# Kernel tuning notes

Hardware: AMD Instinct MI355X
Metric: run time of the kernel (lower is better)

The kernel has to match this reference:

```python
import jax, jax.numpy as jnp
import numpy as np

N_NODES = 100000
N_EDGES = 1600000
D_IN = 128
D_HID = 128
D_OUT = 128
N_GRAPHS = 64


def setup_inputs() -> dict:
    key = jax.random.key(0)
    ks = jax.random.split(key, 10)
    x = jax.random.normal(ks[0], (N_NODES, D_IN), dtype=jnp.float32)
    edge_index = jax.random.randint(ks[1], (2, N_EDGES), 0, N_NODES, dtype=jnp.int64)
    graph_id = jnp.sort(jax.random.randint(ks[2], (N_NODES,), 0, N_GRAPHS, dtype=jnp.int64))
    s1 = 1.0 / np.sqrt(D_IN)
    s2 = 1.0 / np.sqrt(D_HID)
    s3 = 1.0 / np.sqrt(D_OUT)
    W1 = jax.random.normal(ks[3], (D_IN, D_HID), dtype=jnp.float32) * s1
    b1 = jnp.zeros((D_HID,), dtype=jnp.float32)
    W2 = jax.random.normal(ks[4], (D_HID, D_OUT), dtype=jnp.float32) * s2
    b2 = jnp.zeros((D_OUT,), dtype=jnp.float32)
    Wr1 = jax.random.normal(ks[5], (D_OUT, D_OUT), dtype=jnp.float32) * s3
    br1 = jnp.zeros((D_OUT,), dtype=jnp.float32)
    Wr2 = jax.random.normal(ks[6], (D_OUT, D_OUT), dtype=jnp.float32) * s3
    br2 = jnp.zeros((D_OUT,), dtype=jnp.float32)
    return {"x": x, "edge_index": edge_index, "graph_id": graph_id,
            "num_graphs": N_GRAPHS, "W1": W1, "b1": b1, "W2": W2, "b2": b2,
            "Wr1": Wr1, "br1": br1, "Wr2": Wr2, "br2": br2}


def _graph_conv(h, W, b, src, dst, norm_src, norm_dst, n_nodes):
    # DGL GraphConv, norm='both': out = D_dst^{-1/2} A (D_src^{-1/2} h) W + b
    h = h * norm_src[:, None]
    h = h @ W  # project first (cheap, keeps SpMM on the smaller/equal dim)
    agg = jax.ops.segment_sum(h[src], dst, num_segments=n_nodes)
    return agg * norm_dst[:, None] + b


def reference(x, edge_index, graph_id, num_graphs, W1, b1, W2, b2, Wr1, br1, Wr2, br2):
    src, dst = edge_index[0], edge_index[1]
    n_nodes = x.shape[0]
    ones = jnp.ones((src.shape[0],), dtype=x.dtype)
    deg_out = jax.ops.segment_sum(ones, src, num_segments=n_nodes)
    deg_in = jax.ops.segment_sum(ones, dst, num_segments=n_nodes)
    norm_src = jnp.clip(deg_out, 1.0) ** -0.5
    norm_dst = jnp.clip(deg_in, 1.0) ** -0.5

    # layer 1 + relu (dropout is identity in eval mode)
    h = _graph_conv(x, W1, b1, src, dst, norm_src, norm_dst, n_nodes)
    h = jax.nn.relu(h)
    # layer 2 + relu
    h = _graph_conv(h, W2, b2, src, dst, norm_src, norm_dst, n_nodes)
    h = jax.nn.relu(h)

    # per-graph mean pooling (dgl.mean_nodes)
    sums = jax.ops.segment_sum(h, graph_id, num_segments=num_graphs)
    counts = jax.ops.segment_sum(jnp.ones((n_nodes,), dtype=h.dtype), graph_id,
                                 num_segments=num_graphs)
    hg = sums / jnp.clip(counts, 1.0)[:, None]

    # readout MLP: Linear -> ReLU -> Linear
    out = jax.nn.relu(hg @ Wr1 + br1) @ Wr2 + br2
    return (out, h)
```

## Files before the change

kernel.cpp:

```cpp
#include <hip/hip_runtime.h>
#include <math.h>


#define D 128
#define BSH 8
#define BKT 256
#define CAP 4608
#define SCHUNK 3200

typedef _Float16 half8 __attribute__((ext_vector_type(8)));
typedef _Float16 half4v __attribute__((ext_vector_type(4)));
typedef _Float16 half2v __attribute__((ext_vector_type(2)));
typedef float f32x4 __attribute__((ext_vector_type(4)));

union H8 { half8 v; half2v h[4]; };

__global__ __launch_bounds__(512) void k_build(const int* __restrict__ src,
                                               const int* __restrict__ dst,
                                               int* __restrict__ cnt_d,
                                               int* __restrict__ cnt_s,
                                               int* __restrict__ packed_d,
                                               int* __restrict__ packed_s,
                                               int E, int nbkt) {
  __shared__ int es[SCHUNK], ed[SCHUNK];
  __shared__ int hd[512], hs[512], based[512], bases[512];
  int t = threadIdx.x;
  hd[t] = 0; hs[t] = 0;
  __syncthreads();
  int chunk = (E + gridDim.x - 1) / gridDim.x;
  int lo = blockIdx.x * chunk, hi = min(lo + chunk, E);
  int n = hi - lo;
  for (int i = t; i < n; i += 512) {
    int s = src[lo + i], d = dst[lo + i];
    es[i] = s; ed[i] = d;
    atomicAdd(&hd[d >> BSH], 1);
    atomicAdd(&hs[s >> BSH], 1);
  }
  __syncthreads();
  int cD = (t < nbkt) ? hd[t] : 0;
  int cS = (t < nbkt) ? hs[t] : 0;
  __syncthreads();
  hd[t] = 0; hs[t] = 0;
  if (t < nbkt) {
    based[t] = cD ? atomicAdd(&cnt_d[t], cD) : 0;
    bases[t] = cS ? atomicAdd(&cnt_s[t], cS) : 0;
  }
  __syncthreads();
  for (int i = t; i < n; i += 512) {
    int s = es[i], d = ed[i];
    int b1 = d >> BSH;
    int p1 = based[b1] + atomicAdd(&hd[b1], 1);
    if (p1 < CAP) packed_d[b1 * CAP + p1] = ((d & (BKT - 1)) << 17) | s;
    int b2 = s >> BSH;
    int p2 = bases[b2] + atomicAdd(&hs[b2], 1);
    if (p2 < CAP) packed_s[b2 * CAP + p2] = s & (BKT - 1);
  }
}

__global__ __launch_bounds__(512) void k_fine(const int* __restrict__ packed_d,
                                              const int* __restrict__ cnt_d,
                                              int* __restrict__ row_lo,
                                              int* __restrict__ row_hi,
                                              int* __restrict__ csr,
                                              const int* __restrict__ packed_s,
                                              const int* __restrict__ cnt_s,
                                              float* __restrict__ norm_src,
                                              int N, int nbkt) {
  __shared__ int hist[256];
  int t = threadIdx.x;
  if (blockIdx.x >= nbkt) {
    int b = blockIdx.x - nbkt;
    int lo = b * CAP;
    int cnt = min(cnt_s[b], CAP);
    if (t < 256) hist[t] = 0;
    __syncthreads();
    for (int e = t; e < cnt; e += 512)
      atomicAdd(&hist[packed_s[lo + e]], 1);
    __syncthreads();
    int nbase = b << BSH;
    if (t < 256 && nbase + t < N)
      norm_src[nbase + t] = rsqrtf(fmaxf((float)hist[t], 1.0f));
    return;
  }
  __shared__ int excl[256];
  __shared__ int ecache[CAP];
  __shared__ int sorted[CAP];
  int b = blockIdx.x;
  int lo = b * CAP;
  int cnt = min(cnt_d[b], CAP);
  if (t < 256) hist[t] = 0;
  __syncthreads();
  for (int e = t; e < cnt; e += 512) {
    int p = packed_d[lo + e];
    ecache[e] = p;
    atomicAdd(&hist[p >> 17], 1);
  }
  __syncthreads();
  int v = (t < 256) ? hist[t] : 0;
  for (int off = 1; off < 256; off <<= 1) {
    int a = (t >= off && t < 256) ? hist[t - off] : 0;
    __syncthreads();
    if (t < 256) hist[t] += a;
    __syncthreads();
  }
  int nbase = b << BSH;
  if (t < 256) {
    excl[t] = hist[t] - v;
    if (nbase + t < N) {
      row_lo[nbase + t] = lo + hist[t] - v;
      row_hi[nbase + t] = lo + hist[t];
    }
  }
  __syncthreads();
  if (t < 256) hist[t] = 0;
  __syncthreads();
  for (int e = t; e < cnt; e += 512) {
    int p = ecache[e];
    int dlow = p >> 17;
    int r = atomicAdd(&hist[dlow], 1);
    sorted[excl[dlow] + r] = p & 0x1FFFF;
  }
  __syncthreads();
  for (int e = t; e < cnt; e += 512)
    csr[lo + e] = sorted[e];
}

__global__ __launch_bounds__(256) void k_prep(const float* __restrict__ W1,
                                              const float* __restrict__ W2,
                                              _Float16* __restrict__ Wt1,
                                              _Float16* __restrict__ Wt2,
                                              int* __restrict__ cnt_d,
                                              float* __restrict__ pool,
                                              const int* __restrict__ gid,
                                              int* __restrict__ gptr, int N) {
  if (blockIdx.x == 128) {
    int t = threadIdx.x;
    cnt_d[t] = 0; cnt_d[t + 256] = 0; cnt_d[t + 512] = 0; cnt_d[t + 768] = 0;
    for (int i = t; i < 64 * D; i += 256) pool[i] = 0.0f;
    if (t <= 64) {
      int lo = 0, hi = N;
      while (lo < hi) {
        int m = (lo + hi) >> 1;
        if (gid[m] < t) lo = m + 1; else hi = m;
      }
      gptr[t] = lo;
    }
    return;
  }
  int idx = blockIdx.x * 256 + threadIdx.x;
  int m = idx >> 14;
  int i = idx & 16383;
  int k = i >> 7, n = i & 127;
  const float* W = m ? W2 : W1;
  _Float16* Wt = m ? Wt2 : Wt1;
  Wt[n * 128 + k] = (_Float16)W[i];
}

__global__ __launch_bounds__(256) void k_gemm1(const float* __restrict__ A,
                                               const _Float16* __restrict__ Wt,
                                               const float* __restrict__ scale,
                                               _Float16* __restrict__ C, int N) {
  __shared__ _Float16 As[64][136];
  __shared__ _Float16 Cs[64][128];
  const int r0 = blockIdx.x * 64;
  const int t = threadIdx.x;
  for (int i = t; i < 64 * 32; i += 256) {
    int r = i >> 5, c4 = i & 31;
    float4 v = {0.f, 0.f, 0.f, 0.f};
    if (r0 + r < N) {
      v = ((const float4*)A)[(size_t)(r0 + r) * 32 + c4];
      float s = scale[r0 + r];
      v.x *= s; v.y *= s; v.z *= s; v.w *= s;
    }
    half4v h = {(_Float16)v.x, (_Float16)v.y, (_Float16)v.z, (_Float16)v.w};
    *(half4v*)&As[r][c4 * 4] = h;
  }
  __syncthreads();
  const int w = t >> 6, l = t & 63;
  const int c = l & 15, quad = l >> 4;
  f32x4 acc[8];
#pragma unroll
  for (int nt = 0; nt < 8; ++nt) acc[nt] = (f32x4){0.f, 0.f, 0.f, 0.f};
#pragma unroll
  for (int kc = 0; kc < 4; ++kc) {
    half8 a = *(const half8*)&As[w * 16 + c][kc * 32 + quad * 8];
#pragma unroll
    for (int nt = 0; nt < 8; ++nt) {
      half8 b = *(const half8*)&Wt[(size_t)(nt * 16 + c) * 128 + kc * 32 + quad * 8];
      acc[nt] = __builtin_amdgcn_mfma_f32_16x16x32_f16(a, b, acc[nt], 0, 0, 0);
    }
  }
#pragma unroll
  for (int nt = 0; nt < 8; ++nt)
#pragma unroll
    for (int r = 0; r < 4; ++r)
      Cs[w * 16 + quad * 4 + r][nt * 16 + c] = (_Float16)acc[nt][r];
  __syncthreads();
  for (int i = t; i < 64 * 16; i += 256) {
    int r = i >> 4, c8 = i & 15;
    if (r0 + r < N)
      ((half8*)C)[(size_t)(r0 + r) * 16 + c8] = *(half8*)&Cs[r][c8 * 8];
  }
}

__global__ __launch_bounds__(256) void k_gemm2(const _Float16* __restrict__ A,
                                               const _Float16* __restrict__ Wt,
                                               _Float16* __restrict__ C, int N) {
  __shared__ _Float16 As[64][136];
  __shared__ _Float16 Cs[64][128];
  const int r0 = blockIdx.x * 64;
  const int t = threadIdx.x;
  for (int i = t; i < 64 * 16; i += 256) {
    int r = i >> 4, c8 = i & 15;
    half8 v = {0, 0, 0, 0, 0, 0, 0, 0};
    if (r0 + r < N) v = ((const half8*)A)[(size_t)(r0 + r) * 16 + c8];
    *(half8*)&As[r][c8 * 8] = v;
  }
  __syncthreads();
  const int w = t >> 6, l = t & 63;
  const int c = l & 15, quad = l >> 4;
  f32x4 acc[8];
#pragma unroll
  for (int nt = 0; nt < 8; ++nt) acc[nt] = (f32x4){0.f, 0.f, 0.f, 0.f};
#pragma unroll
  for (int kc = 0; kc < 4; ++kc) {
    half8 a = *(const half8*)&As[w * 16 + c][kc * 32 + quad * 8];
#pragma unroll
    for (int nt = 0; nt < 8; ++nt) {
      half8 b = *(const half8*)&Wt[(size_t)(nt * 16 + c) * 128 + kc * 32 + quad * 8];
      acc[nt] = __builtin_amdgcn_mfma_f32_16x16x32_f16(a, b, acc[nt], 0, 0, 0);
    }
  }
#pragma unroll
  for (int nt = 0; nt < 8; ++nt)
#pragma unroll
    for (int r = 0; r < 4; ++r)
      Cs[w * 16 + quad * 4 + r][nt * 16 + c] = (_Float16)acc[nt][r];
  __syncthreads();
  for (int i = t; i < 64 * 16; i += 256) {
    int r = i >> 4, c8 = i & 15;
    if (r0 + r < N)
      ((half8*)C)[(size_t)(r0 + r) * 16 + c8] = *(half8*)&Cs[r][c8 * 8];
  }
}

#define PK_ROW(u)                                                           \
  _Pragma("unroll")                                                         \
  for (int k = 0; k < 4; ++k) acch[k] += (u).h[k];

__device__ __forceinline__ void gather_core(const half8* __restrict__ P8,
                                            const int* __restrict__ csr,
                                            int start, int end, int cg, int eg,
                                            int lane, float* acc) {
  half2v acch[4] = {{(_Float16)0.f, (_Float16)0.f}, {(_Float16)0.f, (_Float16)0.f},
                    {(_Float16)0.f, (_Float16)0.f}, {(_Float16)0.f, (_Float16)0.f}};
  for (int s0 = start; s0 < end; s0 += 64) {
    int cnt = min(64, end - s0);
    int idx = (s0 + lane < end) ? csr[s0 + lane] : 0;
    int base = 0;
    for (; base + 16 <= cnt; base += 16) {
      int i0 = __shfl(idx, base + eg);
      int i1 = __shfl(idx, base + 4 + eg);
      int i2 = __shfl(idx, base + 8 + eg);
      int i3 = __shfl(idx, base + 12 + eg);
      H8 u0, u1, u2, u3;
      u0.v = P8[(size_t)i0 * 16 + cg];
      u1.v = P8[(size_t)i1 * 16 + cg];
      u2.v = P8[(size_t)i2 * 16 + cg];
      u3.v = P8[(size_t)i3 * 16 + cg];
      PK_ROW(u0) PK_ROW(u1) PK_ROW(u2) PK_ROW(u3)
    }
    for (; base + 4 <= cnt; base += 4) {
      int i0 = __shfl(idx, base + eg);
      H8 u0;
      u0.v = P8[(size_t)i0 * 16 + cg];
      PK_ROW(u0)
    }
    if (base < cnt) {
      int j = min(base + eg, cnt - 1);
      int i0 = __shfl(idx, j);
      if (base + eg < cnt) {
        H8 u0;
        u0.v = P8[(size_t)i0 * 16 + cg];
        PK_ROW(u0)
      }
    }
  }
#pragma unroll
  for (int k = 0; k < 4; ++k) {
    acc[2 * k]     = (float)acch[k].x;
    acc[2 * k + 1] = (float)acch[k].y;
  }
#pragma unroll
  for (int j = 0; j < 8; ++j) {
    acc[j] += __shfl_xor(acc[j], 16);
    acc[j] += __shfl_xor(acc[j], 32);
  }
}

__global__ __launch_bounds__(256) void k_gather1(const half8* __restrict__ P8,
                                                 const int* __restrict__ row_lo,
                                                 const int* __restrict__ row_hi,
                                                 const int* __restrict__ csr,
                                                 const float* __restrict__ bias,
                                                 const float* __restrict__ norm_src,
                                                 half2v* __restrict__ outH, int N) {
  int wid = (blockIdx.x * 256 + threadIdx.x) >> 6;
  if (wid >= N) return;
  int lane = threadIdx.x & 63;
  int cg = lane & 15, eg = lane >> 4;
  int start = row_lo[wid], end = row_hi[wid];
  float acc[8];
  gather_core(P8, csr, start, end, cg, eg, lane, acc);
  float nd = rsqrtf(fmaxf((float)(end - start), 1.0f));
  float ns = norm_src[wid];
  float2 b = ((const float2*)bias)[cg * 4 + eg];
  half2v o = {(_Float16)(fmaxf(acc[eg * 2] * nd + b.x, 0.f) * ns),
              (_Float16)(fmaxf(acc[eg * 2 + 1] * nd + b.y, 0.f) * ns)};
  outH[(size_t)wid * 64 + cg * 4 + eg] = o;
}

__global__ __launch_bounds__(256) void k_gather2(const half8* __restrict__ P8,
                                                 const int* __restrict__ row_lo,
                                                 const int* __restrict__ row_hi,
                                                 const int* __restrict__ csr,
                                                 const float* __restrict__ bias,
                                                 float2* __restrict__ outH, int N) {
  int wid = (blockIdx.x * 256 + threadIdx.x) >> 6;
  if (wid >= N) return;
  int lane = threadIdx.x & 63;
  int cg = lane & 15, eg = lane >> 4;
  int start = row_lo[wid], end = row_hi[wid];
  float acc[8];
  gather_core(P8, csr, start, end, cg, eg, lane, acc);
  float nd = rsqrtf(fmaxf((float)(end - start), 1.0f));
  float2 b = ((const float2*)bias)[cg * 4 + eg];
  float2 o;
  o.x = fmaxf(acc[eg * 2] * nd + b.x, 0.f);
  o.y = fmaxf(acc[eg * 2 + 1] * nd + b.y, 0.f);
  outH[(size_t)wid * 64 + cg * 4 + eg] = o;
}

__global__ __launch_bounds__(256) void k_pool(const float* __restrict__ H,
                                              const int* __restrict__ gptr,
                                              float* __restrict__ pool) {
  int g = blockIdx.x >> 3, chunk = blockIdx.x & 7;
  int col = threadIdx.x & 127, rpar = threadIdx.x >> 7;
  int s = gptr[g], e = gptr[g + 1];
  float acc = 0.0f;
  for (int r = s + chunk * 2 + rpar; r < e; r += 16)
    acc += H[(size_t)r * D + col];
  __shared__ float red[256];
  red[threadIdx.x] = acc;
  __syncthreads();
  if (rpar == 0) atomicAdd(&pool[g * D + col], acc + red[threadIdx.x + 128]);
}

__global__ __launch_bounds__(128) void k_readout(const float* __restrict__ pool,
                                                 const int* __restrict__ gptr,
                                                 const float* __restrict__ Wr1,
                                                 const float* __restrict__ br1,
                                                 const float* __restrict__ Wr2,
                                                 const float* __restrict__ br2,
                                                 float* __restrict__ out) {
  int g = blockIdx.x;
  int j = threadIdx.x;
  __shared__ float hg[D];
  __shared__ float t1[D];
  float cnt = fmaxf((float)(gptr[g + 1] - gptr[g]), 1.0f);
  hg[j] = pool[(size_t)g * D + j] / cnt;
  __syncthreads();
  float a = br1[j];
  for (int k = 0; k < D; ++k) a += hg[k] * Wr1[(size_t)k * D + j];
  t1[j] = fmaxf(a, 0.0f);
  __syncthreads();
  float b = br2[j];
  for (int k = 0; k < D; ++k) b += t1[k] * Wr2[(size_t)k * D + j];
  out[(size_t)g * D + j] = b;
}

extern "C" void kernel_launch(void* const* d_in, const int* in_sizes, int n_in,
                              void* d_out, int out_size, void* d_ws, size_t ws_size,
                              hipStream_t stream) {
  const float* x   = (const float*)d_in[0];
  const int* edge  = (const int*)d_in[1];
  const int* gid   = (const int*)d_in[2];
  const float* W1  = (const float*)d_in[4];
  const float* b1  = (const float*)d_in[5];
  const float* W2  = (const float*)d_in[6];
  const float* b2  = (const float*)d_in[7];
  const float* Wr1 = (const float*)d_in[8];
  const float* br1 = (const float*)d_in[9];
  const float* Wr2 = (const float*)d_in[10];
  const float* br2 = (const float*)d_in[11];

  const int N = in_sizes[0] / D;
  const int E = in_sizes[1] / 2;
  const int* src = edge;
  const int* dst = edge + E;
  const int nbkt = (N + BKT - 1) >> BSH;

  float* bufA     = (float*)d_ws;
  float* bufB     = bufA + (size_t)N * D;
  int* row_lo     = (int*)(bufB + (size_t)N * D);
  int* row_hi     = row_lo + N;
  int* csr        = row_hi + N;
  float* norm_src = (float*)(csr + (size_t)nbkt * CAP);
  float* pool     = norm_src + N;
  int* gptr       = (int*)(pool + 64 * D);
  int* cnt_d      = gptr + 65;
  int* cnt_s      = cnt_d + 512;
  _Float16* Wt1   = (_Float16*)(cnt_s + 512);
  _Float16* Wt2   = Wt1 + 128 * 128;
  int* packed_d   = (int*)bufA;
  int* packed_s   = packed_d + (size_t)nbkt * CAP;
  size_t need = ((size_t)2 * N * D + 3 * (size_t)N + (size_t)nbkt * CAP
                 + 64 * D + 65 + 1024 + 16384 + 1024) * sizeof(float);
  if (ws_size < need) return;

  float* out_g = (float*)d_out;
  float* h_out = out_g + 64 * D;

  _Float16* P   = (_Float16*)bufA;
  _Float16* h1p = (_Float16*)bufB;

  k_prep<<<129, 256, 0, stream>>>(W1, W2, Wt1, Wt2, cnt_d, pool, gid, gptr, N);

  const int build_grid = (E + SCHUNK - 1) / SCHUNK;
  k_build<<<build_grid, 512, 0, stream>>>(src, dst, cnt_d, cnt_s,
                                          packed_d, packed_s, E, nbkt);
  k_fine<<<2 * nbkt, 512, 0, stream>>>(packed_d, cnt_d, row_lo, row_hi, csr,
                                       packed_s, cnt_s, norm_src, N, nbkt);

  const int gemm_grid = (N + 63) / 64;

  k_gemm1<<<gemm_grid, 256, 0, stream>>>(x, Wt1, norm_src, P, N);
  k_gather1<<<(N * 64 + 255) / 256, 256, 0, stream>>>(
      (const half8*)P, row_lo, row_hi, csr, b1, norm_src, (half2v*)h1p, N);

  k_gemm2<<<gemm_grid, 256, 0, stream>>>(h1p, Wt2, P, N);
  k_gather2<<<(N * 64 + 255) / 256, 256, 0, stream>>>(
      (const half8*)P, row_lo, row_hi, csr, b2, (float2*)h_out, N);

  k_pool<<<64 * 8, 256, 0, stream>>>(h_out, gptr, pool);
  k_readout<<<64, 128, 0, stream>>>(pool, gptr, Wr1, br1, Wr2, br2, out_g);
}
```

Before: 383.3 us.

## Merge graph build and first GEMM into cooperative persistent kernel; fuse pool+readout

Replaces the prep, bucket-build, fine-sort and first GEMM launches with one cooperative persistent kernel that uses grid-wide syncs between phases and a shared-memory union. Pooling and the readout MLP are likewise merged into one cooperative kernel. The aim is to cut kernel launch gaps and tail effects across several small phases. The cost is that phases now run at a limited grid size (at most 1024 blocks of 256 threads instead of 512-thread blocks). Grid syncs and reduced parallelism in the build and sort steps could make those phases slower.

```diff
diff --git a/kernel.cpp b/kernel.cpp
--- a/kernel.cpp
+++ b/kernel.cpp
@@ -1,4 +1,5 @@
 #include <hip/hip_runtime.h>
+#include <hip/hip_cooperative_groups.h>
 #include <math.h>
 
 
@@ -6,7 +7,6 @@
 #define BSH 8
 #define BKT 256
 #define CAP 4608
-#define SCHUNK 3200
 
 typedef _Float16 half8 __attribute__((ext_vector_type(8)));
 typedef _Float16 half4v __attribute__((ext_vector_type(4)));
@@ -15,127 +15,38 @@
 
 union H8 { half8 v; half2v h[4]; };
 
-__global__ __launch_bounds__(512) void k_build(const int* __restrict__ src,
-                                               const int* __restrict__ dst,
-                                               int* __restrict__ cnt_d,
-                                               int* __restrict__ cnt_s,
-                                               int* __restrict__ packed_d,
-                                               int* __restrict__ packed_s,
-                                               int E, int nbkt) {
-  __shared__ int es[SCHUNK], ed[SCHUNK];
-  __shared__ int hd[512], hs[512], based[512], bases[512];
-  int t = threadIdx.x;
-  hd[t] = 0; hs[t] = 0;
-  __syncthreads();
-  int chunk = (E + gridDim.x - 1) / gridDim.x;
-  int lo = blockIdx.x * chunk, hi = min(lo + chunk, E);
-  int n = hi - lo;
-  for (int i = t; i < n; i += 512) {
-    int s = src[lo + i], d = dst[lo + i];
-    es[i] = s; ed[i] = d;
-    atomicAdd(&hd[d >> BSH], 1);
-    atomicAdd(&hs[s >> BSH], 1);
-  }
-  __syncthreads();
-  int cD = (t < nbkt) ? hd[t] : 0;
-  int cS = (t < nbkt) ? hs[t] : 0;
-  __syncthreads();
-  hd[t] = 0; hs[t] = 0;
-  if (t < nbkt) {
-    based[t] = cD ? atomicAdd(&cnt_d[t], cD) : 0;
-    bases[t] = cS ? atomicAdd(&cnt_s[t], cS) : 0;
-  }
-  __syncthreads();
-  for (int i = t; i < n; i += 512) {
-    int s = es[i], d = ed[i];
-    int b1 = d >> BSH;
-    int p1 = based[b1] + atomicAdd(&hd[b1], 1);
-    if (p1 < CAP) packed_d[b1 * CAP + p1] = ((d & (BKT - 1)) << 17) | s;
-    int b2 = s >> BSH;
-    int p2 = bases[b2] + atomicAdd(&hs[b2], 1);
-    if (p2 < CAP) packed_s[b2 * CAP + p2] = s & (BKT - 1);
-  }
-}
-
-__global__ __launch_bounds__(512) void k_fine(const int* __restrict__ packed_d,
-                                              const int* __restrict__ cnt_d,
-                                              int* __restrict__ row_lo,
-                                              int* __restrict__ row_hi,
-                                              int* __restrict__ csr,
-                                              const int* __restrict__ packed_s,
-                                              const int* __restrict__ cnt_s,
-                                              float* __restrict__ norm_src,
-                                              int N, int nbkt) {
-  __shared__ int hist[256];
-  int t = threadIdx.x;
-  if (blockIdx.x >= nbkt) {
-    int b = blockIdx.x - nbkt;
-    int lo = b * CAP;
-    int cnt = min(cnt_s[b], CAP);
-    if (t < 256) hist[t] = 0;
-    __syncthreads();
-    for (int e = t; e < cnt; e += 512)
-      atomicAdd(&hist[packed_s[lo + e]], 1);
-    __syncthreads();
-    int nbase = b << BSH;
-    if (t < 256 && nbase + t < N)
-      norm_src[nbase + t] = rsqrtf(fmaxf((float)hist[t], 1.0f));
-    return;
-  }
-  __shared__ int excl[256];
-  __shared__ int ecache[CAP];
-  __shared__ int sorted[CAP];
-  int b = blockIdx.x;
-  int lo = b * CAP;
-  int cnt = min(cnt_d[b], CAP);
-  if (t < 256) hist[t] = 0;
-  __syncthreads();
-  for (int e = t; e < cnt; e += 512) {
-    int p = packed_d[lo + e];
-    ecache[e] = p;
-    atomicAdd(&hist[p >> 17], 1);
-  }
-  __syncthreads();
-  int v = (t < 256) ? hist[t] : 0;
-  for (int off = 1; off < 256; off <<= 1) {
-    int a = (t >= off && t < 256) ? hist[t - off] : 0;
-    __syncthreads();
-    if (t < 256) hist[t] += a;
-    __syncthreads();
-  }
-  int nbase = b << BSH;
-  if (t < 256) {
-    excl[t] = hist[t] - v;
-    if (nbase + t < N) {
-      row_lo[nbase + t] = lo + hist[t] - v;
-      row_hi[nbase + t] = lo + hist[t];
-    }
-  }
-  __syncthreads();
-  if (t < 256) hist[t] = 0;
-  __syncthreads();
-  for (int e = t; e < cnt; e += 512) {
-    int p = ecache[e];
-    int dlow = p >> 17;
-    int r = atomicAdd(&hist[dlow], 1);
-    sorted[excl[dlow] + r] = p & 0x1FFFF;
-  }
-  __syncthreads();
-  for (int e = t; e < cnt; e += 512)
-    csr[lo + e] = sorted[e];
-}
-
-__global__ __launch_bounds__(256) void k_prep(const float* __restrict__ W1,
-                                              const float* __restrict__ W2,
-                                              _Float16* __restrict__ Wt1,
-                                              _Float16* __restrict__ Wt2,
-                                              int* __restrict__ cnt_d,
-                                              float* __restrict__ pool,
-                                              const int* __restrict__ gid,
-                                              int* __restrict__ gptr, int N) {
-  if (blockIdx.x == 128) {
-    int t = threadIdx.x;
-    cnt_d[t] = 0; cnt_d[t + 256] = 0; cnt_d[t + 512] = 0; cnt_d[t + 768] = 0;
+union BigLds {
+  struct { int hd[512], hs[512], based[512], bases[512]; } b;
+  struct { int hist[256], excl[256], ecache[CAP], sorted[CAP]; } f;
+  struct { int hist[256]; } fs;
+  struct { _Float16 As[64][136]; _Float16 Cs[64][128]; } g;
+};
+
+__global__ __launch_bounds__(256, 4) void k_graph(
+    const float* __restrict__ W1, const float* __restrict__ W2,
+    _Float16* __restrict__ Wt1, _Float16* __restrict__ Wt2,
+    int* __restrict__ cnt_d, int* __restrict__ cnt_s,
+    float* __restrict__ pool, const int* __restrict__ gid,
+    int* __restrict__ gptr,
+    const int* __restrict__ src, const int* __restrict__ dst,
+    int* __restrict__ packed_d, int* __restrict__ packed_s,
+    int* __restrict__ row_lo, int* __restrict__ row_hi,
+    int* __restrict__ csr, float* __restrict__ norm_src,
+    const float* __restrict__ x, _Float16* __restrict__ P,
+    int N, int E, int nbkt) {
+  __shared__ BigLds sh;
+  cooperative_groups::grid_group grid = cooperative_groups::this_grid();
+  const int t = threadIdx.x;
+  const int bid = blockIdx.x;
+  const int G = gridDim.x;
+
+  for (int idx = bid * 256 + t; idx < 2 * 128 * 128; idx += G * 256) {
+    int m = idx >> 14, i = idx & 16383;
+    int k = i >> 7, n = i & 127;
+    (m ? Wt2 : Wt1)[n * 128 + k] = (_Float16)((m ? W2 : W1)[i]);
+  }
+  if (bid == 0) {
+    for (int i = t; i < 1024; i += 256) cnt_d[i] = 0;
     for (int i = t; i < 64 * D; i += 256) pool[i] = 0.0f;
     if (t <= 64) {
       int lo = 0, hi = N;
@@ -145,61 +56,187 @@
       }
       gptr[t] = lo;
     }
-    return;
-  }
-  int idx = blockIdx.x * 256 + threadIdx.x;
-  int m = idx >> 14;
-  int i = idx & 16383;
-  int k = i >> 7, n = i & 127;
-  const float* W = m ? W2 : W1;
-  _Float16* Wt = m ? Wt2 : Wt1;
-  Wt[n * 128 + k] = (_Float16)W[i];
-}
-
-__global__ __launch_bounds__(256) void k_gemm1(const float* __restrict__ A,
-                                               const _Float16* __restrict__ Wt,
-                                               const float* __restrict__ scale,
-                                               _Float16* __restrict__ C, int N) {
-  __shared__ _Float16 As[64][136];
-  __shared__ _Float16 Cs[64][128];
-  const int r0 = blockIdx.x * 64;
+  }
+  grid.sync();
+
+  {
+    sh.b.hd[t] = 0; sh.b.hd[t + 256] = 0;
+    sh.b.hs[t] = 0; sh.b.hs[t + 256] = 0;
+    __syncthreads();
+    int chunk = (E + G - 1) / G;
+    int lo = bid * chunk, hi = min(lo + chunk, E);
+    for (int i = lo + t; i < hi; i += 256) {
+      atomicAdd(&sh.b.hd[dst[i] >> BSH], 1);
+      atomicAdd(&sh.b.hs[src[i] >> BSH], 1);
+    }
+    __syncthreads();
+    int c0d = sh.b.hd[t], c1d = sh.b.hd[t + 256];
+    int c0s = sh.b.hs[t], c1s = sh.b.hs[t + 256];
+    __syncthreads();
+    sh.b.hd[t] = 0; sh.b.hd[t + 256] = 0;
+    sh.b.hs[t] = 0; sh.b.hs[t + 256] = 0;
+    if (t < nbkt)       sh.b.based[t]       = c0d ? atomicAdd(&cnt_d[t], c0d) : 0;
+    if (t + 256 < nbkt) sh.b.based[t + 256] = c1d ? atomicAdd(&cnt_d[t + 256], c1d) : 0;
+    if (t < nbkt)       sh.b.bases[t]       = c0s ? atomicAdd(&cnt_s[t], c0s) : 0;
+    if (t + 256 < nbkt) sh.b.bases[t + 256] = c1s ? atomicAdd(&cnt_s[t + 256], c1s) : 0;
+    __syncthreads();
+    for (int i = lo + t; i < hi; i += 256) {
+      int s = src[i], d = dst[i];
+      int b1 = d >> BSH;
+      int p1 = sh.b.based[b1] + atomicAdd(&sh.b.hd[b1], 1);
+      if (p1 < CAP) packed_d[b1 * CAP + p1] = ((d & (BKT - 1)) << 17) | s;
+      int b2 = s >> BSH;
+      int p2 = sh.b.bases[b2] + atomicAdd(&sh.b.hs[b2], 1);
+      if (p2 < CAP) packed_s[b2 * CAP + p2] = s & (BKT - 1);
+    }
+  }
+  grid.sync();
+
+  for (int task = bid; task < 2 * nbkt; task += G) {
+    if (task >= nbkt) {
+      int b = task - nbkt;
+      int lo = b * CAP;
+      int cnt = min(cnt_s[b], CAP);
+      sh.fs.hist[t] = 0;
+      __syncthreads();
+      for (int e = t; e < cnt; e += 256)
+        atomicAdd(&sh.fs.hist[packed_s[lo + e]], 1);
+      __syncthreads();
+      int nbase = b << BSH;
+      if (nbase + t < N)
+        norm_src[nbase + t] = rsqrtf(fmaxf((float)sh.fs.hist[t], 1.0f));
+      __syncthreads();
+    } else {
+      int b = task;
+      int lo = b * CAP;
+      int cnt = min(cnt_d[b], CAP);
+      sh.f.hist[t] = 0;
+      __syncthreads();
+      for (int e = t; e < cnt; e += 256) {
+        int p = packed_d[lo + e];
+        sh.f.ecache[e] = p;
+        atomicAdd(&sh.f.hist[p >> 17], 1);
+      }
+      __syncthreads();
+      int v = sh.f.hist[t];
+      for (int off = 1; off < 256; off <<= 1) {
+        int a = (t >= off) ? sh.f.hist[t - off] : 0;
+        __syncthreads();
+        sh.f.hist[t] += a;
+        __syncthreads();
+      }
+      sh.f.excl[t] = sh.f.hist[t] - v;
+      int nbase = b << BSH;
+      if (nbase + t < N) {
+        row_lo[nbase + t] = lo + sh.f.hist[t] - v;
+        row_hi[nbase + t] = lo + sh.f.hist[t];
+      }
+      __syncthreads();
+      sh.f.hist[t] = 0;
+      __syncthreads();
+      for (int e = t; e < cnt; e += 256) {
+        int p = sh.f.ecache[e];
+        int dlow = p >> 17;
+        int r = atomicAdd(&sh.f.hist[dlow], 1);
+        sh.f.sorted[sh.f.excl[dlow] + r] = p & 0x1FFFF;
+      }
+      __syncthreads();
+      for (int e = t; e < cnt; e += 256)
+        csr[lo + e] = sh.f.sorted[e];
+      __syncthreads();
+    }
+  }
+  grid.sync();
+
+  {
+    const int ntiles = (N + 63) >> 6;
+    const int w = t >> 6, l = t & 63;
+    const int c = l & 15, quad = l >> 4;
+    for (int tile = bid; tile < ntiles; tile += G) {
+      const int r0 = tile * 64;
+      for (int i = t; i < 64 * 32; i += 256) {
+        int r = i >> 5, c4 = i & 31;
+        float4 v = {0.f, 0.f, 0.f, 0.f};
+        if (r0 + r < N) {
+          v = ((const float4*)x)[(size_t)(r0 + r) * 32 + c4];
+          float s = norm_src[r0 + r];
+          v.x *= s; v.y *= s; v.z *= s; v.w *= s;
+        }
+        half4v h = {(_Float16)v.x, (_Float16)v.y, (_Float16)v.z, (_Float16)v.w};
+        *(half4v*)&sh.g.As[r][c4 * 4] = h;
+      }
+      __syncthreads();
+      f32x4 acc[8];
+#pragma unroll
+      for (int nt = 0; nt < 8; ++nt) acc[nt] = (f32x4){0.f, 0.f, 0.f, 0.f};
+#pragma unroll
+      for (int kc = 0; kc < 4; ++kc) {
+        half8 a = *(const half8*)&sh.g.As[w * 16 + c][kc * 32 + quad * 8];
+#pragma unroll
+        for (int nt = 0; nt < 8; ++nt) {
+          half8 b = *(const half8*)&Wt1[(size_t)(nt * 16 + c) * 128 + kc * 32 + quad * 8];
+          acc[nt] = __builtin_amdgcn_mfma_f32_16x16x32_f16(a, b, acc[nt], 0, 0, 0);
+        }
+      }
+#pragma unroll
+      for (int nt = 0; nt < 8; ++nt)
+#pragma unroll
+        for (int r = 0; r < 4; ++r)
+          sh.g.Cs[w * 16 + quad * 4 + r][nt * 16 + c] = (_Float16)acc[nt][r];
+      __syncthreads();
+      for (int i = t; i < 64 * 16; i += 256) {
+        int r = i >> 4, c8 = i & 15;
+        if (r0 + r < N)
+          ((half8*)P)[(size_t)(r0 + r) * 16 + c8] = *(half8*)&sh.g.Cs[r][c8 * 8];
+      }
+      __syncthreads();
+    }
+  }
+}
+
+__global__ __launch_bounds__(256, 2) void k_tail(
+    const float* __restrict__ H, const int* __restrict__ gptr,
+    float* __restrict__ pool,
+    const float* __restrict__ Wr1, const float* __restrict__ br1,
+    const float* __restrict__ Wr2, const float* __restrict__ br2,
+    float* __restrict__ out) {
+  cooperative_groups::grid_group grid = cooperative_groups::this_grid();
   const int t = threadIdx.x;
-  for (int i = t; i < 64 * 32; i += 256) {
-    int r = i >> 5, c4 = i & 31;
-    float4 v = {0.f, 0.f, 0.f, 0.f};
-    if (r0 + r < N) {
-      v = ((const float4*)A)[(size_t)(r0 + r) * 32 + c4];
-      float s = scale[r0 + r];
-      v.x *= s; v.y *= s; v.z *= s; v.w *= s;
-    }
-    half4v h = {(_Float16)v.x, (_Float16)v.y, (_Float16)v.z, (_Float16)v.w};
-    *(half4v*)&As[r][c4 * 4] = h;
-  }
-  __syncthreads();
-  const int w = t >> 6, l = t & 63;
-  const int c = l & 15, quad = l >> 4;
-  f32x4 acc[8];
-#pragma unroll
-  for (int nt = 0; nt < 8; ++nt) acc[nt] = (f32x4){0.f, 0.f, 0.f, 0.f};
-#pragma unroll
-  for (int kc = 0; kc < 4; ++kc) {
-    half8 a = *(const half8*)&As[w * 16 + c][kc * 32 + quad * 8];
-#pragma unroll
-    for (int nt = 0; nt < 8; ++nt) {
-      half8 b = *(const half8*)&Wt[(size_t)(nt * 16 + c) * 128 + kc * 32 + quad * 8];
-      acc[nt] = __builtin_amdgcn_mfma_f32_16x16x32_f16(a, b, acc[nt], 0, 0, 0);
-    }
-  }
-#pragma unroll
-  for (int nt = 0; nt < 8; ++nt)
-#pragma unroll
-    for (int r = 0; r < 4; ++r)
-      Cs[w * 16 + quad * 4 + r][nt * 16 + c] = (_Float16)acc[nt][r];
-  __syncthreads();
-  for (int i = t; i < 64 * 16; i += 256) {
-    int r = i >> 4, c8 = i & 15;
-    if (r0 + r < N)
-      ((half8*)C)[(size_t)(r0 + r) * 16 + c8] = *(half8*)&Cs[r][c8 * 8];
+  const int bid = blockIdx.x;
+  const int G = gridDim.x;
+  __shared__ float red[256];
+  __shared__ float hg[128];
+  __shared__ float t1[128];
+
+  for (int task = bid; task < 512; task += G) {
+    int g = task >> 3, chunk = task & 7;
+    int col = t & 127, rpar = t >> 7;
+    int s = gptr[g], e = gptr[g + 1];
+    float acc = 0.0f;
+    for (int r = s + chunk * 2 + rpar; r < e; r += 16)
+      acc += H[(size_t)r * D + col];
+    red[t] = acc;
+    __syncthreads();
+    if (rpar == 0) atomicAdd(&pool[g * D + col], acc + red[t + 128]);
+    __syncthreads();
+  }
+  grid.sync();
+  for (int g = bid; g < 64; g += G) {
+    float cnt = fmaxf((float)(gptr[g + 1] - gptr[g]), 1.0f);
+    if (t < 128) hg[t] = pool[(size_t)g * D + t] / cnt;
+    __syncthreads();
+    if (t < 128) {
+      float a = br1[t];
+      for (int k = 0; k < D; ++k) a += hg[k] * Wr1[(size_t)k * D + t];
+      t1[t] = fmaxf(a, 0.0f);
+    }
+    __syncthreads();
+    if (t < 128) {
+      float b = br2[t];
+      for (int k = 0; k < D; ++k) b += t1[k] * Wr2[(size_t)k * D + t];
+      out[(size_t)g * D + t] = b;
+    }
+    __syncthreads();
   }
 }
 
@@ -341,44 +378,6 @@
   outH[(size_t)wid * 64 + cg * 4 + eg] = o;
 }
 
-__global__ __launch_bounds__(256) void k_pool(const float* __restrict__ H,
-                                              const int* __restrict__ gptr,
-                                              float* __restrict__ pool) {
-  int g = blockIdx.x >> 3, chunk = blockIdx.x & 7;
-  int col = threadIdx.x & 127, rpar = threadIdx.x >> 7;
-  int s = gptr[g], e = gptr[g + 1];
-  float acc = 0.0f;
-  for (int r = s + chunk * 2 + rpar; r < e; r += 16)
-    acc += H[(size_t)r * D + col];
-  __shared__ float red[256];
-  red[threadIdx.x] = acc;
-  __syncthreads();
-  if (rpar == 0) atomicAdd(&pool[g * D + col], acc + red[threadIdx.x + 128]);
-}
-
-__global__ __launch_bounds__(128) void k_readout(const float* __restrict__ pool,
-                                                 const int* __restrict__ gptr,
-                                                 const float* __restrict__ Wr1,
-                                                 const float* __restrict__ br1,
-                                                 const float* __restrict__ Wr2,
-                                                 const float* __restrict__ br2,
-                                                 float* __restrict__ out) {
-  int g = blockIdx.x;
-  int j = threadIdx.x;
-  __shared__ float hg[D];
-  __shared__ float t1[D];
-  float cnt = fmaxf((float)(gptr[g + 1] - gptr[g]), 1.0f);
-  hg[j] = pool[(size_t)g * D + j] / cnt;
-  __syncthreads();
-  float a = br1[j];
-  for (int k = 0; k < D; ++k) a += hg[k] * Wr1[(size_t)k * D + j];
-  t1[j] = fmaxf(a, 0.0f);
-  __syncthreads();
-  float b = br2[j];
-  for (int k = 0; k < D; ++k) b += t1[k] * Wr2[(size_t)k * D + j];
-  out[(size_t)g * D + j] = b;
-}
-
 extern "C" void kernel_launch(void* const* d_in, const int* in_sizes, int n_in,
                               void* d_out, int out_size, void* d_ws, size_t ws_size,
                               hipStream_t stream) {
@@ -424,24 +423,44 @@
   _Float16* P   = (_Float16*)bufA;
   _Float16* h1p = (_Float16*)bufB;
 
-  k_prep<<<129, 256, 0, stream>>>(W1, W2, Wt1, Wt2, cnt_d, pool, gid, gptr, N);
-
-  const int build_grid = (E + SCHUNK - 1) / SCHUNK;
-  k_build<<<build_grid, 512, 0, stream>>>(src, dst, cnt_d, cnt_s,
-                                          packed_d, packed_s, E, nbkt);
-  k_fine<<<2 * nbkt, 512, 0, stream>>>(packed_d, cnt_d, row_lo, row_hi, csr,
-                                       packed_s, cnt_s, norm_src, N, nbkt);
-
-  const int gemm_grid = (N + 63) / 64;
-
-  k_gemm1<<<gemm_grid, 256, 0, stream>>>(x, Wt1, norm_src, P, N);
+  static int G1 = 0, G2 = 0;
+  if (G1 == 0) {
+    int occ1 = 0, occ2 = 0, ncu = 256;
+    hipOccupancyMaxActiveBlocksPerMultiprocessor(&occ1, k_graph, 256, 0);
+    hipOccupancyMaxActiveBlocksPerMultiprocessor(&occ2, k_tail, 256, 0);
+    hipDeviceProp_t prop;
+    int dev = 0;
+    if (hipGetDevice(&dev) == hipSuccess &&
+        hipGetDeviceProperties(&prop, dev) == hipSuccess &&
+        prop.multiProcessorCount > 0)
+      ncu = prop.multiProcessorCount;
+    G1 = (occ1 > 0) ? min(1024, occ1 * ncu) : 1024;
+    G2 = (occ2 > 0) ? min(512, occ2 * ncu) : 512;
+  }
+
+  {
+    int n_ = N, e_ = E, nb_ = nbkt;
+    void* args[] = {
+      (void*)&W1, (void*)&W2, (void*)&Wt1, (void*)&Wt2,
+      (void*)&cnt_d, (void*)&cnt_s, (void*)&pool, (void*)&gid, (void*)&gptr,
+      (void*)&src, (void*)&dst, (void*)&packed_d, (void*)&packed_s,
+      (void*)&row_lo, (void*)&row_hi, (void*)&csr, (void*)&norm_src,
+      (void*)&x, (void*)&P, (void*)&n_, (void*)&e_, (void*)&nb_};
+    hipLaunchCooperativeKernel(k_graph, dim3(G1), dim3(256), args, 0, stream);
+  }
+
   k_gather1<<<(N * 64 + 255) / 256, 256, 0, stream>>>(
       (const half8*)P, row_lo, row_hi, csr, b1, norm_src, (half2v*)h1p, N);
 
+  const int gemm_grid = (N + 63) / 64;
   k_gemm2<<<gemm_grid, 256, 0, stream>>>(h1p, Wt2, P, N);
   k_gather2<<<(N * 64 + 255) / 256, 256, 0, stream>>>(
       (const half8*)P, row_lo, row_hi, csr, b2, (float2*)h_out, N);
 
-  k_pool<<<64 * 8, 256, 0, stream>>>(h_out, gptr, pool);
-  k_readout<<<64, 128, 0, stream>>>(pool, gptr, Wr1, br1, Wr2, br2, out_g);
-}
+  {
+    void* args[] = {
+      (void*)&h_out, (void*)&gptr, (void*)&pool,
+      (void*)&Wr1, (void*)&br1, (void*)&Wr2, (void*)&br2, (void*)&out_g};
+    hipLaunchCooperativeKernel(k_tail, dim3(G2), dim3(256), args, 0, stream);
+  }
+}
```

After: 681.2 us. +77.7%, slower.

## Fold weight prep into edge-binning kernel and drop shared edge staging

Applied to the files above, without the earlier changes.

Removes the separate k_prep launch. Its work moves into k_build: the weight transpose to fp16 and the graph-pointer binary search. The counter and pool zeroing becomes hipMemsetAsync calls. k_build now runs a fixed grid of 1024 blocks of 256 threads and reads src/dst twice from global memory, where before it staged about 3200 edges per block in LDS. The aim is to cut one launch and the LDS pressure that limited occupancy. The cost is a second global read of the edge arrays and two extra memset operations.

```diff
diff --git a/kernel.cpp b/kernel.cpp
--- a/kernel.cpp
+++ b/kernel.cpp
@@ -6,7 +6,7 @@
 #define BSH 8
 #define BKT 256
 #define CAP 4608
-#define SCHUNK 3200
+#define BGRID 1024
 
 typedef _Float16 half8 __attribute__((ext_vector_type(8)));
 typedef _Float16 half4v __attribute__((ext_vector_type(4)));
@@ -15,39 +15,59 @@
 
 union H8 { half8 v; half2v h[4]; };
 
-__global__ __launch_bounds__(512) void k_build(const int* __restrict__ src,
+__global__ __launch_bounds__(256) void k_build(const int* __restrict__ src,
                                                const int* __restrict__ dst,
                                                int* __restrict__ cnt_d,
                                                int* __restrict__ cnt_s,
                                                int* __restrict__ packed_d,
                                                int* __restrict__ packed_s,
-                                               int E, int nbkt) {
-  __shared__ int es[SCHUNK], ed[SCHUNK];
+                                               const float* __restrict__ W1,
+                                               const float* __restrict__ W2,
+                                               _Float16* __restrict__ Wt1,
+                                               _Float16* __restrict__ Wt2,
+                                               const int* __restrict__ gid,
+                                               int* __restrict__ gptr,
+                                               int N, int E, int nbkt) {
   __shared__ int hd[512], hs[512], based[512], bases[512];
-  int t = threadIdx.x;
-  hd[t] = 0; hs[t] = 0;
+  const int t = threadIdx.x;
+  const int bid = blockIdx.x;
+
+  for (int idx = bid * 256 + t; idx < 2 * 128 * 128; idx += gridDim.x * 256) {
+    int m = idx >> 14, i = idx & 16383;
+    int k = i >> 7, n = i & 127;
+    (m ? Wt2 : Wt1)[n * 128 + k] = (_Float16)((m ? W2 : W1)[i]);
+  }
+  if (bid == gridDim.x - 1 && t <= 64) {
+    int lo = 0, hi = N;
+    while (lo < hi) {
+      int m = (lo + hi) >> 1;
+      if (gid[m] < t) lo = m + 1; else hi = m;
+    }
+    gptr[t] = lo;
+  }
+
+  hd[t] = 0; hd[t + 256] = 0;
+  hs[t] = 0; hs[t + 256] = 0;
   __syncthreads();
   int chunk = (E + gridDim.x - 1) / gridDim.x;
-  int lo = blockIdx.x * chunk, hi = min(lo + chunk, E);
-  int n = hi - lo;
-  for (int i = t; i < n; i += 512) {
-    int s = src[lo + i], d = dst[lo + i];
-    es[i] = s; ed[i] = d;
-    atomicAdd(&hd[d >> BSH], 1);
-    atomicAdd(&hs[s >> BSH], 1);
-  }
-  __syncthreads();
-  int cD = (t < nbkt) ? hd[t] : 0;
-  int cS = (t < nbkt) ? hs[t] : 0;
-  __syncthreads();
-  hd[t] = 0; hs[t] = 0;
-  if (t < nbkt) {
-    based[t] = cD ? atomicAdd(&cnt_d[t], cD) : 0;
-    bases[t] = cS ? atomicAdd(&cnt_s[t], cS) : 0;
-  }
-  __syncthreads();
-  for (int i = t; i < n; i += 512) {
-    int s = es[i], d = ed[i];
+  int lo = bid * chunk, hi = min(lo + chunk, E);
+  for (int i = lo + t; i < hi; i += 256) {
+    atomicAdd(&hd[dst[i] >> BSH], 1);
+    atomicAdd(&hs[src[i] >> BSH], 1);
+  }
+  __syncthreads();
+  int c0d = hd[t], c1d = hd[t + 256];
+  int c0s = hs[t], c1s = hs[t + 256];
+  __syncthreads();
+  hd[t] = 0; hd[t + 256] = 0;
+  hs[t] = 0; hs[t + 256] = 0;
+  if (t < nbkt)       based[t]       = c0d ? atomicAdd(&cnt_d[t], c0d) : 0;
+  if (t + 256 < nbkt) based[t + 256] = c1d ? atomicAdd(&cnt_d[t + 256], c1d) : 0;
+  if (t < nbkt)       bases[t]       = c0s ? atomicAdd(&cnt_s[t], c0s) : 0;
+  if (t + 256 < nbkt) bases[t + 256] = c1s ? atomicAdd(&cnt_s[t + 256], c1s) : 0;
+  __syncthreads();
+  for (int i = lo + t; i < hi; i += 256) {
+    int s = src[i], d = dst[i];
     int b1 = d >> BSH;
     int p1 = based[b1] + atomicAdd(&hd[b1], 1);
     if (p1 < CAP) packed_d[b1 * CAP + p1] = ((d & (BKT - 1)) << 17) | s;
@@ -125,37 +145,6 @@
     csr[lo + e] = sorted[e];
 }
 
-__global__ __launch_bounds__(256) void k_prep(const float* __restrict__ W1,
-                                              const float* __restrict__ W2,
-                                              _Float16* __restrict__ Wt1,
-                                              _Float16* __restrict__ Wt2,
-                                              int* __restrict__ cnt_d,
-                                              float* __restrict__ pool,
-                                              const int* __restrict__ gid,
-                                              int* __restrict__ gptr, int N) {
-  if (blockIdx.x == 128) {
-    int t = threadIdx.x;
-    cnt_d[t] = 0; cnt_d[t + 256] = 0; cnt_d[t + 512] = 0; cnt_d[t + 768] = 0;
-    for (int i = t; i < 64 * D; i += 256) pool[i] = 0.0f;
-    if (t <= 64) {
-      int lo = 0, hi = N;
-      while (lo < hi) {
-        int m = (lo + hi) >> 1;
-        if (gid[m] < t) lo = m + 1; else hi = m;
-      }
-      gptr[t] = lo;
-    }
-    return;
-  }
-  int idx = blockIdx.x * 256 + threadIdx.x;
-  int m = idx >> 14;
-  int i = idx & 16383;
-  int k = i >> 7, n = i & 127;
-  const float* W = m ? W2 : W1;
-  _Float16* Wt = m ? Wt2 : Wt1;
-  Wt[n * 128 + k] = (_Float16)W[i];
-}
-
 __global__ __launch_bounds__(256) void k_gemm1(const float* __restrict__ A,
                                                const _Float16* __restrict__ Wt,
                                                const float* __restrict__ scale,
@@ -424,11 +413,11 @@
   _Float16* P   = (_Float16*)bufA;
   _Float16* h1p = (_Float16*)bufB;
 
-  k_prep<<<129, 256, 0, stream>>>(W1, W2, Wt1, Wt2, cnt_d, pool, gid, gptr, N);
-
-  const int build_grid = (E + SCHUNK - 1) / SCHUNK;
-  k_build<<<build_grid, 512, 0, stream>>>(src, dst, cnt_d, cnt_s,
-                                          packed_d, packed_s, E, nbkt);
+  hipMemsetAsync(cnt_d, 0, 1024 * sizeof(int), stream);
+  hipMemsetAsync(pool, 0, 64 * D * sizeof(float), stream);
+
+  k_build<<<BGRID, 256, 0, stream>>>(src, dst, cnt_d, cnt_s, packed_d, packed_s,
+                                     W1, W2, Wt1, Wt2, gid, gptr, N, E, nbkt);
   k_fine<<<2 * nbkt, 512, 0, stream>>>(packed_d, cnt_d, row_lo, row_hi, csr,
                                        packed_s, cnt_s, norm_src, N, nbkt);
 
```

Result: slower. 418.7 us (+9.2%).
